# Kernel tuning notes

Measured on AMD Instinct MI355X. Metric: run time of the kernel, lower is better.

## Reference

```python
import jax, jax.numpy as jnp
import numpy as np

NUM_FINE = 1048576
NUM_FEATURES = 128
TARGET_NUM_SEGMENTS = 262144


def setup_inputs() -> dict:
    key = jax.random.key(0)
    k1, k2 = jax.random.split(key)
    fine_scale_h_d = jax.random.normal(k1, (NUM_FINE, NUM_FEATURES), dtype=jnp.float32)
    prolongation_map_fine_to_coarse = jax.random.randint(
        k2, (NUM_FINE,), 0, TARGET_NUM_SEGMENTS, dtype=jnp.int32)
    return {
        "fine_scale_h_d": fine_scale_h_d,
        "prolongation_map_fine_to_coarse": prolongation_map_fine_to_coarse,
    }


def reference(fine_scale_h_d, prolongation_map_fine_to_coarse):
    # segment_mean = segment_sum / segment_count, with 0 for empty segments
    # (matches tf.math.segment_mean). No sort needed: segment_sum handles
    # unsorted ids via scatter-add, which is the math-equivalent single pass.
    seg_sum = jax.ops.segment_sum(
        fine_scale_h_d, prolongation_map_fine_to_coarse,
        num_segments=TARGET_NUM_SEGMENTS)  # [S, F]
    seg_cnt = jax.ops.segment_sum(
        jnp.ones((fine_scale_h_d.shape[0],), dtype=fine_scale_h_d.dtype),
        prolongation_map_fine_to_coarse,
        num_segments=TARGET_NUM_SEGMENTS)  # [S]
    denom = jnp.maximum(seg_cnt, 1.0)[:, None]
    return seg_sum / denom
```

## Files before the change

kernel.cpp:

```cpp
#include <hip/hip_runtime.h>

#define NUM_FINE 1048576
#define NF 128
#define NUM_SEG 262144

typedef float f32x4 __attribute__((ext_vector_type(4)));

__global__ void count_rank_kernel(const int* __restrict__ ids, int* __restrict__ cnt,
                                  int* __restrict__ rank) {
    int i = (blockIdx.x * blockDim.x + threadIdx.x) * 4;
    int4 a = *reinterpret_cast<const int4*>(ids + i);
    int4 r;
    r.x = atomicAdd(&cnt[a.x], 1);
    r.y = atomicAdd(&cnt[a.y], 1);
    r.z = atomicAdd(&cnt[a.z], 1);
    r.w = atomicAdd(&cnt[a.w], 1);
    *reinterpret_cast<int4*>(rank + i) = r;
}

__global__ void scan1_kernel(const int* __restrict__ cnt, int* __restrict__ base,
                             int* __restrict__ blockSums) {
    __shared__ int lds[256];
    int tid = threadIdx.x;
    int g = blockIdx.x * 1024 + tid * 4;
    int4 a = *reinterpret_cast<const int4*>(cnt + g);
    int s = a.x + a.y + a.z + a.w;
    lds[tid] = s;
    __syncthreads();
    for (int off = 1; off < 256; off <<= 1) {
        int v = (tid >= off) ? lds[tid - off] : 0;
        __syncthreads();
        lds[tid] += v;
        __syncthreads();
    }
    int excl = lds[tid] - s;
    int4 o;
    o.x = excl;
    o.y = o.x + a.x;
    o.z = o.y + a.y;
    o.w = o.z + a.z;
    *reinterpret_cast<int4*>(base + g) = o;
    if (tid == 255) blockSums[blockIdx.x] = lds[255];
}

__global__ void scan3_kernel(int* __restrict__ base, const int* __restrict__ blockSums,
                             const int* __restrict__ cnt, int2* __restrict__ desc) {
    __shared__ int lds[256];
    int tid = threadIdx.x;
    int v = blockSums[tid];
    lds[tid] = v;
    __syncthreads();
    for (int off = 1; off < 256; off <<= 1) {
        int t = (tid >= off) ? lds[tid - off] : 0;
        __syncthreads();
        lds[tid] += t;
        __syncthreads();
    }
    int add = (blockIdx.x > 0) ? lds[blockIdx.x - 1] : 0;
    int g = blockIdx.x * 1024 + tid * 4;
    int4 b = *reinterpret_cast<int4*>(base + g);
    int4 cc = *reinterpret_cast<const int4*>(cnt + g);
    b.x += add; b.y += add; b.z += add; b.w += add;
    *reinterpret_cast<int4*>(base + g) = b;
    *reinterpret_cast<int4*>(desc + g)     = make_int4(b.x, cc.x, b.y, cc.y);
    *reinterpret_cast<int4*>(desc + g + 2) = make_int4(b.z, cc.z, b.w, cc.w);
}

__global__ void place_kernel(const int* __restrict__ ids, const int* __restrict__ base,
                             const int* __restrict__ rank, int* __restrict__ perm) {
    int i = (blockIdx.x * blockDim.x + threadIdx.x) * 4;
    int4 a = *reinterpret_cast<const int4*>(ids + i);
    int4 r = *reinterpret_cast<const int4*>(rank + i);
    perm[base[a.x] + r.x] = i;
    perm[base[a.y] + r.y] = i + 1;
    perm[base[a.z] + r.z] = i + 2;
    perm[base[a.w] + r.w] = i + 3;
}

__device__ __forceinline__ f32x4 rowx(const float* __restrict__ x, int row, int f) {
    return *reinterpret_cast<const f32x4*>(x + (size_t)row * NF + f);
}

__global__ void gather_kernel(const float* __restrict__ x,
                              const int* __restrict__ perm,
                              const int2* __restrict__ desc,
                              float* __restrict__ out) {
    int wid = (blockIdx.x << 2) | (threadIdx.x >> 6);
    int lane = threadIdx.x & 63;
    int h = lane >> 5;
    int f = (lane & 31) << 2;
    int2 d = desc[wid];
    int start = d.x, c = d.y;
    f32x4 acc = {0.f, 0.f, 0.f, 0.f};
    if (c > 0) {
        int pl = lane & 7;
        int pv = perm[start + ((pl < c) ? pl : (c - 1))];
        int r0 = __shfl(pv, h);
        if (c <= 2) {
            f32x4 v0 = rowx(x, r0, f);
            float m0 = (h < c) ? 1.f : 0.f;
            acc = v0 * m0;
        } else if (c <= 4) {
            int r1 = __shfl(pv, 2 + h);
            f32x4 v0 = rowx(x, r0, f);
            f32x4 v1 = rowx(x, r1, f);
            float m1 = (2 + h < c) ? 1.f : 0.f;
            acc = v0 + v1 * m1;
        } else if (c <= 6) {
            int r1 = __shfl(pv, 2 + h);
            int r2 = __shfl(pv, 4 + h);
            f32x4 v0 = rowx(x, r0, f);
            f32x4 v1 = rowx(x, r1, f);
            f32x4 v2 = rowx(x, r2, f);
            float m2 = (4 + h < c) ? 1.f : 0.f;
            acc = v0 + v1 + v2 * m2;
        } else if (c <= 8) {
            int r1 = __shfl(pv, 2 + h);
            int r2 = __shfl(pv, 4 + h);
            int r3 = __shfl(pv, 6 + h);
            f32x4 v0 = rowx(x, r0, f);
            f32x4 v1 = rowx(x, r1, f);
            f32x4 v2 = rowx(x, r2, f);
            f32x4 v3 = rowx(x, r3, f);
            float m3 = (6 + h < c) ? 1.f : 0.f;
            acc = v0 + v1 + v2 + v3 * m3;
        } else {
            int end = start + c;
            for (int r = start; r < end; r += 8) {
                int pj = r + pl;
                pv = perm[(pj < end) ? pj : (end - 1)];
                int q0 = __shfl(pv, h);
                int q1 = __shfl(pv, 2 + h);
                int q2 = __shfl(pv, 4 + h);
                int q3 = __shfl(pv, 6 + h);
                f32x4 v0 = rowx(x, q0, f);
                f32x4 v1 = rowx(x, q1, f);
                f32x4 v2 = rowx(x, q2, f);
                f32x4 v3 = rowx(x, q3, f);
                int rem = end - r;
                float m0 = (h < rem)     ? 1.f : 0.f;
                float m1 = (2 + h < rem) ? 1.f : 0.f;
                float m2 = (4 + h < rem) ? 1.f : 0.f;
                float m3 = (6 + h < rem) ? 1.f : 0.f;
                acc += v0 * m0 + v1 * m1 + v2 * m2 + v3 * m3;
            }
        }
        acc.x += __shfl_xor(acc.x, 32);
        acc.y += __shfl_xor(acc.y, 32);
        acc.z += __shfl_xor(acc.z, 32);
        acc.w += __shfl_xor(acc.w, 32);
    }
    if (h == 0) {
        float inv = 1.0f / (float)(c > 1 ? c : 1);
        f32x4 o = acc * inv;
        *reinterpret_cast<f32x4*>(out + (size_t)wid * NF + f) = o;
    }
}

extern "C" void kernel_launch(void* const* d_in, const int* in_sizes, int n_in,
                              void* d_out, int out_size, void* d_ws, size_t ws_size,
                              hipStream_t stream) {
    const float* x   = (const float*)d_in[0];
    const int*   ids = (const int*)d_in[1];
    float* out = (float*)d_out;

    char* ws = (char*)d_ws;
    int*  cnt       = (int*)(ws);
    int*  base      = (int*)(ws + (1 << 20));
    int*  blockSums = (int*)(ws + (2 << 20));
    int*  perm      = (int*)(ws + (3 << 20));
    int*  rank      = (int*)(ws + (7 << 20));
    int2* desc      = (int2*)(ws + (11 << 20));

    hipMemsetAsync(cnt, 0, (size_t)NUM_SEG * sizeof(int), stream);

    count_rank_kernel<<<NUM_FINE / 1024, 256, 0, stream>>>(ids, cnt, rank);
    scan1_kernel<<<NUM_SEG / 1024, 256, 0, stream>>>(cnt, base, blockSums);
    scan3_kernel<<<NUM_SEG / 1024, 256, 0, stream>>>(base, blockSums, cnt, desc);
    place_kernel<<<NUM_FINE / 1024, 256, 0, stream>>>(ids, base, rank, perm);

    gather_kernel<<<NUM_SEG / 4, 256, 0, stream>>>(x, perm, desc, out);
}
```

Baseline: 207.4 us.

## Fuse two-pass scan into single kernel with inter-block spin-wait publication

Merges the block-local scan and the block-sum propagation into one kernel. Each block publishes its total (offset by one) to a zeroed array, and every block spin-waits on all 256 totals before adding its prefix. This removes one launch and the round trip of the base array through memory. The placement kernel now reads base offsets from the interleaved desc array. The change relies on all 256 blocks being co-resident, which holds on this GPU but is not guaranteed by the programming model, and the memset now also clears the publication area.

```diff
diff --git a/kernel.cpp b/kernel.cpp
--- a/kernel.cpp
+++ b/kernel.cpp
@@ -18,11 +18,11 @@
     *reinterpret_cast<int4*>(rank + i) = r;
 }
 
-__global__ void scan1_kernel(const int* __restrict__ cnt, int* __restrict__ base,
-                             int* __restrict__ blockSums) {
+__global__ void scan_fused(const int* __restrict__ cnt, int* __restrict__ pub,
+                           int2* __restrict__ desc) {
     __shared__ int lds[256];
-    int tid = threadIdx.x;
-    int g = blockIdx.x * 1024 + tid * 4;
+    int tid = threadIdx.x, bid = blockIdx.x;
+    int g = bid * 1024 + tid * 4;
     int4 a = *reinterpret_cast<const int4*>(cnt + g);
     int s = a.x + a.y + a.z + a.w;
     lds[tid] = s;
@@ -34,20 +34,11 @@
         __syncthreads();
     }
     int excl = lds[tid] - s;
-    int4 o;
-    o.x = excl;
-    o.y = o.x + a.x;
-    o.z = o.y + a.y;
-    o.w = o.z + a.z;
-    *reinterpret_cast<int4*>(base + g) = o;
-    if (tid == 255) blockSums[blockIdx.x] = lds[255];
-}
-
-__global__ void scan3_kernel(int* __restrict__ base, const int* __restrict__ blockSums,
-                             const int* __restrict__ cnt, int2* __restrict__ desc) {
-    __shared__ int lds[256];
-    int tid = threadIdx.x;
-    int v = blockSums[tid];
+    if (tid == 0) atomicExch(&pub[bid], lds[255] + 1);
+    int v;
+    while ((v = atomicAdd(&pub[tid], 0)) == 0) { }
+    v -= 1;
+    __syncthreads();
     lds[tid] = v;
     __syncthreads();
     for (int off = 1; off < 256; off <<= 1) {
@@ -56,25 +47,22 @@
         lds[tid] += t;
         __syncthreads();
     }
-    int add = (blockIdx.x > 0) ? lds[blockIdx.x - 1] : 0;
-    int g = blockIdx.x * 1024 + tid * 4;
-    int4 b = *reinterpret_cast<int4*>(base + g);
-    int4 cc = *reinterpret_cast<const int4*>(cnt + g);
-    b.x += add; b.y += add; b.z += add; b.w += add;
-    *reinterpret_cast<int4*>(base + g) = b;
-    *reinterpret_cast<int4*>(desc + g)     = make_int4(b.x, cc.x, b.y, cc.y);
-    *reinterpret_cast<int4*>(desc + g + 2) = make_int4(b.z, cc.z, b.w, cc.w);
+    int add = (bid > 0) ? lds[bid - 1] : 0;
+    int b0 = excl + add;
+    int b1 = b0 + a.x, b2 = b1 + a.y, b3 = b2 + a.z;
+    *reinterpret_cast<int4*>(desc + g)     = make_int4(b0, a.x, b1, a.y);
+    *reinterpret_cast<int4*>(desc + g + 2) = make_int4(b2, a.z, b3, a.w);
 }
 
-__global__ void place_kernel(const int* __restrict__ ids, const int* __restrict__ base,
+__global__ void place_kernel(const int* __restrict__ ids, const int2* __restrict__ desc,
                              const int* __restrict__ rank, int* __restrict__ perm) {
     int i = (blockIdx.x * blockDim.x + threadIdx.x) * 4;
     int4 a = *reinterpret_cast<const int4*>(ids + i);
     int4 r = *reinterpret_cast<const int4*>(rank + i);
-    perm[base[a.x] + r.x] = i;
-    perm[base[a.y] + r.y] = i + 1;
-    perm[base[a.z] + r.z] = i + 2;
-    perm[base[a.w] + r.w] = i + 3;
+    perm[desc[a.x].x + r.x] = i;
+    perm[desc[a.y].x + r.y] = i + 1;
+    perm[desc[a.z].x + r.z] = i + 2;
+    perm[desc[a.w].x + r.w] = i + 3;
 }
 
 __device__ __forceinline__ f32x4 rowx(const float* __restrict__ x, int row, int f) {
@@ -165,19 +153,17 @@
     float* out = (float*)d_out;
 
     char* ws = (char*)d_ws;
-    int*  cnt       = (int*)(ws);
-    int*  base      = (int*)(ws + (1 << 20));
-    int*  blockSums = (int*)(ws + (2 << 20));
-    int*  perm      = (int*)(ws + (3 << 20));
-    int*  rank      = (int*)(ws + (7 << 20));
-    int2* desc      = (int2*)(ws + (11 << 20));
+    int*  cnt  = (int*)(ws);
+    int*  pub  = (int*)(ws + (1 << 20));
+    int2* desc = (int2*)(ws + (2 << 20));
+    int*  perm = (int*)(ws + (4 << 20));
+    int*  rank = (int*)(ws + (8 << 20));
 
-    hipMemsetAsync(cnt, 0, (size_t)NUM_SEG * sizeof(int), stream);
+    hipMemsetAsync(cnt, 0, (1 << 20) + 4096, stream);
 
     count_rank_kernel<<<NUM_FINE / 1024, 256, 0, stream>>>(ids, cnt, rank);
-    scan1_kernel<<<NUM_SEG / 1024, 256, 0, stream>>>(cnt, base, blockSums);
-    scan3_kernel<<<NUM_SEG / 1024, 256, 0, stream>>>(base, blockSums, cnt, desc);
-    place_kernel<<<NUM_FINE / 1024, 256, 0, stream>>>(ids, base, rank, perm);
+    scan_fused<<<256, 256, 0, stream>>>(cnt, pub, desc);
+    place_kernel<<<NUM_FINE / 1024, 256, 0, stream>>>(ids, desc, rank, perm);
 
     gather_kernel<<<NUM_SEG / 4, 256, 0, stream>>>(x, perm, desc, out);
 }
```

New measurement: 208.0 us. About the same (+0.3%).
